# Performance work log

Hardware: AMD Instinct MI355X
Metric: run time of the kernel (lower is better)

The kernel has to match this reference:

```python
import jax, jax.numpy as jnp
import numpy as np

NUM_FEATURES = 256
NUM_PIDS = 5532
NUM_CQ = 5000
OIM_SCALAR = 30.0
IGNORE_INDEX = 5554  # roi_label 5555 -> label 5554 -> ignored by cross_entropy
N = 8192
UNLABELED_FRAC = 0.3


def _l2norm(x):
    return x / jnp.linalg.norm(x, axis=-1, keepdims=True)


def setup_inputs() -> dict:
    key = jax.random.key(0)
    k1, k2, k3, k4, k5 = jax.random.split(key, 5)
    inputs = _l2norm(jax.random.normal(k1, (N, NUM_FEATURES), dtype=jnp.float32))
    # roi_label values are 1..num_pids for labeled persons, 5555 for unlabeled;
    # all >= 1 so the `label >= 0` filter in the torch module keeps every row
    # (keeps shapes static / jit-friendly while matching the math exactly).
    labels = jax.random.randint(k2, (N,), 1, NUM_PIDS + 1, dtype=jnp.int32)
    unlabeled = jax.random.uniform(k3, (N,)) < UNLABELED_FRAC
    roi_label = jnp.where(unlabeled, IGNORE_INDEX + 1, labels).astype(jnp.int32)
    lut = _l2norm(jax.random.normal(k4, (NUM_PIDS, NUM_FEATURES), dtype=jnp.float32))
    cq = _l2norm(jax.random.normal(k5, (NUM_CQ, NUM_FEATURES), dtype=jnp.float32))
    return {"inputs": inputs, "roi_label": roi_label, "lut": lut, "cq": cq}


def reference(inputs, roi_label, lut, cq):
    # targets = cat(roi_label); label = targets - 1; inds = label >= 0 keeps all rows here
    label = roi_label - 1  # [N], values in [0, NUM_PIDS-1] or IGNORE_INDEX
    # OIMSMR.forward: projected = [inputs @ lut.T | inputs @ cq.T]
    logits = jnp.concatenate([inputs @ lut.T, inputs @ cq.T], axis=1)  # [N, P+Q]
    logits = logits * OIM_SCALAR
    # cross_entropy with ignore_index=5554 (mean over non-ignored samples)
    valid = label != IGNORE_INDEX
    safe_label = jnp.clip(label, 0, logits.shape[1] - 1)
    logp = jax.nn.log_softmax(logits, axis=1)  # [N, P+Q]
    nll = -jnp.take_along_axis(logp, safe_label[:, None], axis=1)[:, 0]  # [N]
    n_valid = jnp.maximum(jnp.sum(valid.astype(jnp.float32)), 1.0)
    loss = jnp.sum(jnp.where(valid, nll, 0.0)) / n_valid
    return loss
```

## Files before the change

kernel.cpp:

```cpp
#include <hip/hip_runtime.h>
#include <hip/hip_bf16.h>
#include <cstdint>
#include <cstddef>

#define N_ROWS 8192
#define K_DIM  256
#define NP     5532
#define NC     10532
#define NCPAD  10752
#define IGN    5554
#define BM     128
#define BN     128
#define BK     64
#define CT     84
#define NBLK   (CT * 64)
#define CPX    (NBLK / 8)

using f32x4 = __attribute__((ext_vector_type(4))) float;

__global__ __launch_bounds__(256) void oim_convert(
    const float* __restrict__ X, const float* __restrict__ lut,
    const float* __restrict__ cq,
    unsigned char* __restrict__ Xb, unsigned char* __restrict__ Wb)
{
    const int XCH = (N_ROWS * K_DIM) / 8;
    const int WCH = (NCPAD * K_DIM) / 8;
    int c = blockIdx.x * 256 + threadIdx.x;
    if (c >= XCH + WCH) return;
    const float* src = nullptr;
    unsigned char* dst;
    if (c < XCH) {
        src = X + (size_t)c * 8;
        dst = Xb + (size_t)c * 8;
    } else {
        int wc  = c - XCH;
        int row = wc >> 5;
        int off = (wc & 31) * 8;
        dst = Wb + (size_t)wc * 8;
        if (row < NP)      src = lut + (size_t)row * K_DIM + off;
        else if (row < NC) src = cq + (size_t)(row - NP) * K_DIM + off;
    }
    unsigned int lo = 0, hi = 0;
    if (src) {
        float4 v0 = *reinterpret_cast<const float4*>(src);
        float4 v1 = *reinterpret_cast<const float4*>(src + 4);
        lo = __builtin_amdgcn_cvt_pk_fp8_f32(v0.x, v0.y, 0,  false);
        lo = __builtin_amdgcn_cvt_pk_fp8_f32(v0.z, v0.w, lo, true);
        hi = __builtin_amdgcn_cvt_pk_fp8_f32(v1.x, v1.y, 0,  false);
        hi = __builtin_amdgcn_cvt_pk_fp8_f32(v1.z, v1.w, hi, true);
    }
    uint2 o; o.x = lo; o.y = hi;
    *reinterpret_cast<uint2*>(dst) = o;
}

__global__ __launch_bounds__(256, 4) void oim_gemm(
    const unsigned char* __restrict__ Xb, const unsigned char* __restrict__ Wb,
    const int* __restrict__ roi,
    float* __restrict__ partial, float* __restrict__ labelLogit)
{
    const int bid = blockIdx.x;
    const int L   = (bid & 7) * CPX + (bid >> 3);
    const int ct  = L >> 6;
    const int rt  = L & 63;
    const int row0 = rt * BM;
    const int col0 = ct * BN;
    const int tid  = threadIdx.x;
    const int wave = tid >> 6;
    const int lane = tid & 63;
    const int wm   = (wave >> 1) * 64;
    const int wn   = (wave & 1) * 64;

    __shared__ __align__(16) unsigned char As[BM * BK];
    __shared__ __align__(16) unsigned char Bs[BN * BK];
    __shared__ int   lbl[BM];
    __shared__ float rs[BM][2];

    if (tid < BM) lbl[tid] = roi[row0 + tid] - 1;

    const unsigned char* aP[2];
    const unsigned char* bP[2];
#pragma unroll
    for (int i = 0; i < 2; ++i) {
        int c  = i * 256 + tid;
        int r  = ((c >> 3) << 1) | ((c >> 2) & 1);
        int gq = (c & 3) ^ ((c >> 3) & 3);
        aP[i] = Xb + (size_t)(row0 + r) * K_DIM + gq * 16;
        bP[i] = Wb + (size_t)(col0 + r) * K_DIM + gq * 16;
    }

    const int rA = wm + (lane & 15);
    const int rB = wn + (lane & 15);
    const int gs = lane >> 4;
    const int swA = (rA >> 1) & 3, swB = (rB >> 1) & 3;
    const int aBse = ((rA >> 1) << 7) + ((rA & 1) << 6) + ((gs & 1) << 3);
    const int bBse = ((rB >> 1) << 7) + ((rB & 1) << 6) + ((gs & 1) << 3);
    const int aO0 = aBse + ((((gs >> 1))     ^ swA) << 4);
    const int aO1 = aBse + ((((gs >> 1) + 2) ^ swA) << 4);
    const int bO0 = bBse + ((((gs >> 1))     ^ swB) << 4);
    const int bO1 = bBse + ((((gs >> 1) + 2) ^ swB) << 4);

    f32x4 acc[4][4] = {};
    long av0[4], av1[4], bv0[4], bv1[4];

    auto ldsread = [&]() {
#pragma unroll
        for (int m = 0; m < 4; ++m) {
            av0[m] = *reinterpret_cast<const long*>(As + aO0 + m * 1024);
            av1[m] = *reinterpret_cast<const long*>(As + aO1 + m * 1024);
        }
#pragma unroll
        for (int n = 0; n < 4; ++n) {
            bv0[n] = *reinterpret_cast<const long*>(Bs + bO0 + n * 1024);
            bv1[n] = *reinterpret_cast<const long*>(Bs + bO1 + n * 1024);
        }
    };
    auto mfma = [&]() {
#pragma unroll
        for (int m = 0; m < 4; ++m)
#pragma unroll
            for (int n = 0; n < 4; ++n)
                acc[m][n] = __builtin_amdgcn_mfma_f32_16x16x32_fp8_fp8(
                    av0[m], bv0[n], acc[m][n], 0, 0, 0);
#pragma unroll
        for (int m = 0; m < 4; ++m)
#pragma unroll
            for (int n = 0; n < 4; ++n)
                acc[m][n] = __builtin_amdgcn_mfma_f32_16x16x32_fp8_fp8(
                    av1[m], bv1[n], acc[m][n], 0, 0, 0);
    };

#define STAGE(T)                                                              \
    do {                                                                      \
        __builtin_amdgcn_global_load_lds(                                     \
            (const __attribute__((address_space(1))) void*)aP[0],             \
            (__attribute__((address_space(3))) void*)                         \
                ((char*)As + wave * 1024), 16, (T) * 64, 0);                  \
        __builtin_amdgcn_global_load_lds(                                     \
            (const __attribute__((address_space(1))) void*)aP[1],             \
            (__attribute__((address_space(3))) void*)                         \
                ((char*)As + 4096 + wave * 1024), 16, (T) * 64, 0);           \
        __builtin_amdgcn_global_load_lds(                                     \
            (const __attribute__((address_space(1))) void*)bP[0],             \
            (__attribute__((address_space(3))) void*)                         \
                ((char*)Bs + wave * 1024), 16, (T) * 64, 0);                  \
        __builtin_amdgcn_global_load_lds(                                     \
            (const __attribute__((address_space(1))) void*)bP[1],             \
            (__attribute__((address_space(3))) void*)                         \
                ((char*)Bs + 4096 + wave * 1024), 16, (T) * 64, 0);           \
    } while (0)

#define ITER(T)                                                               \
    do {                                                                      \
        ldsread();                                                            \
        __syncthreads();       \
        STAGE((T) + 1);        \
        mfma();                \
        __syncthreads();       \
    } while (0)

    STAGE(0);
    __syncthreads();
    ITER(0); ITER(1); ITER(2);
    ldsread();
    mfma();
#undef ITER
#undef STAGE

#pragma unroll
    for (int m = 0; m < 4; ++m) {
#pragma unroll
        for (int reg = 0; reg < 4; ++reg) {
            int lrow = wm + m * 16 + (lane >> 4) * 4 + reg;
            int grow = row0 + lrow;
            int lab  = lbl[lrow];
            float s = 0.0f;
#pragma unroll
            for (int n = 0; n < 4; ++n) {
                int gcol = col0 + wn + n * 16 + (lane & 15);
                float logit = acc[m][n][reg] * 30.0f;
                s += __expf(logit - 30.0f);
                if (gcol == lab) labelLogit[grow] = logit;
            }
#pragma unroll
            for (int off = 1; off < 16; off <<= 1) s += __shfl_xor(s, off, 64);
            if ((lane & 15) == 0) rs[lrow][wave & 1] = s;
        }
    }
    __syncthreads();
    if (tid < BM)
        partial[(size_t)ct * N_ROWS + row0 + tid] = rs[tid][0] + rs[tid][1];
}

__global__ __launch_bounds__(256) void oim_rownll(
    const float* __restrict__ partial, const float* __restrict__ labelLogit,
    const int* __restrict__ roi, float* __restrict__ blksum)
{
    __shared__ float s1[256], s2[256];
    int tid = threadIdx.x;
    int r = blockIdx.x * 256 + tid;
    float S = 0.0f;
    for (int t = 0; t < CT; ++t) S += partial[(size_t)t * N_ROWS + r];
    float lse = 30.0f + logf(S);
    int lab = roi[r] - 1;
    bool valid = (lab != IGN);
    s1[tid] = valid ? (lse - labelLogit[r]) : 0.0f;
    s2[tid] = valid ? 1.0f : 0.0f;
    __syncthreads();
    for (int o = 128; o > 0; o >>= 1) {
        if (tid < o) { s1[tid] += s1[tid + o]; s2[tid] += s2[tid + o]; }
        __syncthreads();
    }
    if (tid == 0) {
        blksum[blockIdx.x]      = s1[0];
        blksum[32 + blockIdx.x] = s2[0];
    }
}

__global__ __launch_bounds__(64) void oim_reduce(
    const float* __restrict__ blksum, float* __restrict__ out)
{
    int tid = threadIdx.x;
    float a = (tid < 32) ? blksum[tid]      : 0.0f;
    float b = (tid < 32) ? blksum[32 + tid] : 0.0f;
#pragma unroll
    for (int off = 32; off > 0; off >>= 1) {
        a += __shfl_xor(a, off, 64);
        b += __shfl_xor(b, off, 64);
    }
    if (tid == 0) out[0] = a / fmaxf(b, 1.0f);
}

extern "C" void kernel_launch(void* const* d_in, const int* in_sizes, int n_in,
                              void* d_out, int out_size, void* d_ws, size_t ws_size,
                              hipStream_t stream)
{
    const float* X   = (const float*)d_in[0];
    const int*   roi = (const int*)  d_in[1];
    const float* lut = (const float*)d_in[2];
    const float* cq  = (const float*)d_in[3];
    float* out = (float*)d_out;

    char* ws = (char*)d_ws;
    unsigned char* Xb = (unsigned char*)ws;
    unsigned char* Wb = Xb + (size_t)N_ROWS * K_DIM;
    float* partial    = (float*)(Wb + (size_t)NCPAD * K_DIM);
    float* labelLogit = partial + (size_t)CT * N_ROWS;
    float* blksum     = labelLogit + N_ROWS;
    size_t need = (size_t)N_ROWS * K_DIM + (size_t)NCPAD * K_DIM
                + (size_t)CT * N_ROWS * 4 + (size_t)(N_ROWS + 64) * 4;
    if (ws_size < need) return;

    const int TOT_CHUNKS = ((N_ROWS + NCPAD) * K_DIM) / 8;
    oim_convert<<<(TOT_CHUNKS + 255) / 256, 256, 0, stream>>>(X, lut, cq, Xb, Wb);
    oim_gemm<<<NBLK, 256, 0, stream>>>(Xb, Wb, roi, partial, labelLogit);
    oim_rownll<<<N_ROWS / 256, 256, 0, stream>>>(partial, labelLogit, roi, blksum);
    oim_reduce<<<1, 64, 0, stream>>>(blksum, out);
}
```

Measured before the change: 72.60 us.

## Permute FP8 K layout during conversion so GEMM uses 128-bit LDS reads

The conversion kernel now writes each FP8 row with a permuted K ordering, so the two 8-byte MFMA operands a lane needs for the two K halves sit next to each other. The GEMM then replaces two 64-bit LDS reads per fragment with one 128-bit read, halving LDS read instructions and simplifying address arithmetic. It depends on the global-to-LDS staging and the swizzle staying consistent with the new layout, and since both operands are permuted the same way along K the dot products are unchanged.

```diff
diff --git a/kernel.cpp b/kernel.cpp
--- a/kernel.cpp
+++ b/kernel.cpp
@@ -17,6 +17,7 @@
 #define CPX    (NBLK / 8)
 
 using f32x4 = __attribute__((ext_vector_type(4))) float;
+using i64x2 = __attribute__((ext_vector_type(2))) long;
 
 __global__ __launch_bounds__(256) void oim_convert(
     const float* __restrict__ X, const float* __restrict__ lut,
@@ -29,17 +30,19 @@
     if (c >= XCH + WCH) return;
     const float* src = nullptr;
     unsigned char* dst;
+    int row, qg;
     if (c < XCH) {
+        row = c >> 5; qg = c & 31;
         src = X + (size_t)c * 8;
-        dst = Xb + (size_t)c * 8;
+        dst = Xb + (size_t)row * K_DIM;
     } else {
-        int wc  = c - XCH;
-        int row = wc >> 5;
-        int off = (wc & 31) * 8;
-        dst = Wb + (size_t)wc * 8;
-        if (row < NP)      src = lut + (size_t)row * K_DIM + off;
-        else if (row < NC) src = cq + (size_t)(row - NP) * K_DIM + off;
-    }
+        int wc = c - XCH;
+        row = wc >> 5; qg = wc & 31;
+        dst = Wb + (size_t)row * K_DIM;
+        if (row < NP)      src = lut + (size_t)row * K_DIM + qg * 8;
+        else if (row < NC) src = cq + (size_t)(row - NP) * K_DIM + qg * 8;
+    }
+    dst += (qg >> 3) * 64 + (qg & 3) * 16 + ((qg >> 2) & 1) * 8;
     unsigned int lo = 0, hi = 0;
     if (src) {
         float4 v0 = *reinterpret_cast<const float4*>(src);
@@ -90,14 +93,11 @@
 
     const int rA = wm + (lane & 15);
     const int rB = wn + (lane & 15);
-    const int gs = lane >> 4;
-    const int swA = (rA >> 1) & 3, swB = (rB >> 1) & 3;
-    const int aBse = ((rA >> 1) << 7) + ((rA & 1) << 6) + ((gs & 1) << 3);
-    const int bBse = ((rB >> 1) << 7) + ((rB & 1) << 6) + ((gs & 1) << 3);
-    const int aO0 = aBse + ((((gs >> 1))     ^ swA) << 4);
-    const int aO1 = aBse + ((((gs >> 1) + 2) ^ swA) << 4);
-    const int bO0 = bBse + ((((gs >> 1))     ^ swB) << 4);
-    const int bO1 = bBse + ((((gs >> 1) + 2) ^ swB) << 4);
+    const int gK = lane >> 4;
+    const int aOff = ((rA >> 1) << 7) + ((rA & 1) << 6)
+                   + ((gK ^ ((rA >> 1) & 3)) << 4);
+    const int bOff = ((rB >> 1) << 7) + ((rB & 1) << 6)
+                   + ((gK ^ ((rB >> 1) & 3)) << 4);
 
     f32x4 acc[4][4] = {};
     long av0[4], av1[4], bv0[4], bv1[4];
@@ -105,13 +105,13 @@
     auto ldsread = [&]() {
 #pragma unroll
         for (int m = 0; m < 4; ++m) {
-            av0[m] = *reinterpret_cast<const long*>(As + aO0 + m * 1024);
-            av1[m] = *reinterpret_cast<const long*>(As + aO1 + m * 1024);
+            i64x2 v = *reinterpret_cast<const i64x2*>(As + aOff + m * 1024);
+            av0[m] = v.x; av1[m] = v.y;
         }
 #pragma unroll
         for (int n = 0; n < 4; ++n) {
-            bv0[n] = *reinterpret_cast<const long*>(Bs + bO0 + n * 1024);
-            bv1[n] = *reinterpret_cast<const long*>(Bs + bO1 + n * 1024);
+            i64x2 v = *reinterpret_cast<const i64x2*>(Bs + bOff + n * 1024);
+            bv0[n] = v.x; bv1[n] = v.y;
         }
     };
     auto mfma = [&]() {
```

Result: faster. 65.24 us (-10.1%).
